# Performance work log

Hardware: AMD Instinct MI355X
Metric: run time of the kernel (lower is better)

Reference implementation:

```python
import jax, jax.numpy as jnp
import numpy as np

B, N_LEAVES, HID, NCLS, VOCAB = 32, 512, 128, 2, 50257
N_NODES = 2 * N_LEAVES - 1  # complete binary tree, heap layout


def setup_inputs() -> dict:
    key = jax.random.key(0)
    ks = jax.random.split(key, 12)
    x = jax.random.randint(ks[0], (B, N_NODES), 0, VOCAB)
    cue = jax.random.randint(ks[1], (B, N_NODES), 0, NCLS)
    # word j sits at tree leaf node L-1+j
    word_index = jnp.tile(jnp.arange(N_LEAVES - 1, 2 * N_LEAVES - 1), (B, 1))
    # parent->child adjacency stored in adj[:, 1]
    A = np.zeros((2, N_NODES, N_NODES), dtype=bool)
    p = np.arange(N_LEAVES - 1)
    A[1, p, 2 * p + 1] = True
    A[1, p, 2 * p + 2] = True
    adj = jnp.asarray(np.broadcast_to(A, (B, 2, N_NODES, N_NODES)).copy())
    s = 0.05
    emb = jax.random.normal(ks[2], (VOCAB, HID - NCLS)) * s
    Wc = jax.random.normal(ks[3], (HID, 2 * HID)) * s
    bc = jax.random.normal(ks[4], (HID,)) * s
    Wd = jax.random.normal(ks[5], (2 * HID, 2 * HID)) * s
    bd = jax.random.normal(ks[6], (2 * HID,)) * s
    Wg = jax.random.normal(ks[7], (HID, HID)) * s
    bg = jax.random.normal(ks[8], (HID,)) * s
    Wcl = jax.random.normal(ks[9], (NCLS, 2 * HID)) * s
    bcl = jax.random.normal(ks[10], (NCLS,)) * s
    return dict(x=x, word_index=word_index, cue=cue, adj=adj, emb=emb,
                Wc=Wc, bc=bc, Wd=Wd, bd=bd, Wg=Wg, bg=bg, Wcl=Wcl, bcl=bcl)


def reference(x, word_index, cue, adj, emb, Wc, bc, Wd, bd, Wg, bg, Wcl, bcl):
    # adj encodes the same complete binary heap tree that is hardcoded below
    Bn, N = x.shape
    H = Wc.shape[0]
    C = bcl.shape[0]
    L = (N + 1) // 2
    depth = L.bit_length() - 1  # leaves live at level `depth`
    bidx = jnp.arange(Bn)[:, None]

    word_emb = emb[x]                                   # (B, N, H-C)
    cue_oh = jax.nn.one_hot(cue, C, dtype=word_emb.dtype)
    in_feats = jnp.concatenate([word_emb, cue_oh], -1)  # (B, N, H)
    sent = in_feats[bidx, word_index]                   # (B, L, H) leaf feats

    # ---- upward compose: level-batched bottom-up traversal ----
    h = jnp.zeros((Bn, N, H), in_feats.dtype).at[bidx, word_index].set(sent)
    for d in range(depth - 1, -1, -1):
        p = jnp.arange(2 ** d - 1, 2 ** (d + 1) - 1)
        ctx = jnp.concatenate([h[:, 2 * p + 1], h[:, 2 * p + 2]], -1)  # (B, 2^d, 2H)
        h = h.at[:, p].set(jnp.tanh(ctx @ Wc.T + bc))
    # upward_results never writes leaf rows -> leaves stay zero
    up = h.at[bidx, word_index].set(0.0)

    g_down = jax.nn.sigmoid(h[:, 0] @ Wg.T + bg)        # (B, H)

    # ---- downward decompose: level-batched top-down traversal ----
    down = jnp.zeros_like(h).at[:, 0].set(g_down)
    for d in range(depth):
        p = jnp.arange(2 ** d - 1, 2 ** (d + 1) - 1)
        ctx = jnp.concatenate([down[:, p], up[:, p]], -1)
        ch = jnp.tanh(ctx @ Wd.T + bd)                  # (B, 2^d, 2H)
        down = down.at[:, 2 * p + 1].set(ch[..., :H]).at[:, 2 * p + 2].set(ch[..., H:])

    tree = jnp.concatenate([down, up], -1)              # (B, N, 2H)
    scores = jax.nn.sigmoid(tree @ Wcl.T + bcl)
    return jax.nn.softmax(scores, -1)
```

## Files before the change

kernel.cpp:

```cpp
#include <hip/hip_runtime.h>


constexpr int NNODES = 1023;
constexpr int HB = 128;

__device__ __forceinline__ float fold16(const float* a, int l) {
  float b[8];
#pragma unroll
  for (int u = 0; u < 8; ++u) {
    const float mine = (l & 1) ? a[2 * u + 1] : a[2 * u];
    const float oth  = (l & 1) ? a[2 * u]     : a[2 * u + 1];
    b[u] = mine + __shfl_xor(oth, 1);
  }
  float c[4];
#pragma unroll
  for (int u = 0; u < 4; ++u) {
    const float mine = (l & 2) ? b[2 * u + 1] : b[2 * u];
    const float oth  = (l & 2) ? b[2 * u]     : b[2 * u + 1];
    c[u] = mine + __shfl_xor(oth, 2);
  }
  float d[2];
#pragma unroll
  for (int u = 0; u < 2; ++u) {
    const float mine = (l & 4) ? c[2 * u + 1] : c[2 * u];
    const float oth  = (l & 4) ? c[2 * u]     : c[2 * u + 1];
    d[u] = mine + __shfl_xor(oth, 4);
  }
  const float mine = (l & 8) ? d[1] : d[0];
  const float oth  = (l & 8) ? d[0] : d[1];
  return mine + __shfl_xor(oth, 8);
}

__device__ __forceinline__ float fold8(const float* a, int l) {
  float b[4];
#pragma unroll
  for (int u = 0; u < 4; ++u) {
    const float mine = (l & 1) ? a[2 * u + 1] : a[2 * u];
    const float oth  = (l & 1) ? a[2 * u]     : a[2 * u + 1];
    b[u] = mine + __shfl_xor(oth, 1);
  }
  float c[2];
#pragma unroll
  for (int u = 0; u < 2; ++u) {
    const float mine = (l & 2) ? b[2 * u + 1] : b[2 * u];
    const float oth  = (l & 2) ? b[2 * u]     : b[2 * u + 1];
    c[u] = mine + __shfl_xor(oth, 2);
  }
  const float mine = (l & 4) ? c[1] : c[0];
  const float oth  = (l & 4) ? c[0] : c[1];
  return mine + __shfl_xor(oth, 4);
}

__device__ __forceinline__ float fold4(const float* a, int l) {
  float b[2];
#pragma unroll
  for (int u = 0; u < 2; ++u) {
    const float mine = (l & 1) ? a[2 * u + 1] : a[2 * u];
    const float oth  = (l & 1) ? a[2 * u]     : a[2 * u + 1];
    b[u] = mine + __shfl_xor(oth, 1);
  }
  const float mine = (l & 2) ? b[1] : b[0];
  const float oth  = (l & 2) ? b[0] : b[1];
  return mine + __shfl_xor(oth, 2);
}

template<int CH>
__device__ __forceinline__ float foldCH(const float (&a)[CH * 4], int l16) {
  if constexpr (CH == 4) {
    return fold16(a, l16);
  } else if constexpr (CH == 2) {
    float t = fold8(a, l16);
    t += __shfl_xor(t, 8);
    return t;
  } else {
    float t = fold4(a, l16);
    t += __shfl_xor(t, 4);
    t += __shfl_xor(t, 8);
    return t;
  }
}

template<int CH>
__device__ __forceinline__ void up_pass(float* __restrict__ heap, int base, int cb,
                                        int cbase, const float4 (&w)[4][4],
                                        float bias_r, int g, int l16, bool wr) {
  float2 a2[CH * 4];
#pragma unroll
  for (int v = 0; v < CH * 4; ++v) a2[v] = make_float2(0.f, 0.f);
#pragma unroll
  for (int p = 0; p < CH; ++p) {
    const float* cp = heap + (cb + 2 * (cbase + p)) * HB + l16 * 4;
#pragma unroll
    for (int m = 0; m < 4; ++m) {
      const float4 cc = *(const float4*)(cp + m * 64);
#pragma unroll
      for (int r = 0; r < 4; ++r) {
        const float4 wv = w[r][m];
        float2& av = a2[p * 4 + r];
        av.x = fmaf(wv.x, cc.x, av.x);
        av.y = fmaf(wv.y, cc.y, av.y);
        av.x = fmaf(wv.z, cc.z, av.x);
        av.y = fmaf(wv.w, cc.w, av.y);
      }
    }
  }
  float a[CH * 4];
#pragma unroll
  for (int v = 0; v < CH * 4; ++v) a[v] = a2[v].x + a2[v].y;
  const float tot = foldCH<CH>(a, l16);
  if (wr && l16 < CH * 4) {
    const int p = l16 >> 2;
    heap[(base + cbase + p) * HB + 4 * g + (l16 & 3)] = tanhf(tot + bias_r);
  }
}

template<int NP, int NH>
__device__ __forceinline__ void up_level16(float* __restrict__ heap,
                                           const float4 (&w)[4][4],
                                           float bias_r, int g, int l16, int ph) {
  constexpr int base = NP - 1, cb = 2 * NP - 1;
  if constexpr (NP >= 4 * NH) {
#pragma unroll
    for (int c0 = 0; c0 < NP; c0 += 4 * NH)
      up_pass<4>(heap, base, cb, c0 + ph * 4, w, bias_r, g, l16, true);
  } else if constexpr (NP * 2 == 4 * NH) {
    up_pass<2>(heap, base, cb, ph * 2, w, bias_r, g, l16, true);
  } else if constexpr (NP == NH) {
    up_pass<1>(heap, base, cb, ph, w, bias_r, g, l16, true);
  } else {
    up_pass<1>(heap, base, cb, 0, w, bias_r, g, l16, ph == 0);
  }
  __syncthreads();
}

template<int CH>
__device__ __forceinline__ void down_pass(float* __restrict__ db,
                                          const float* __restrict__ ub,
                                          int base, int cb, int cbase,
                                          const float4 (&w)[4][4],
                                          float bias_r, int g, int l16) {
  float2 a2[CH * 4];
#pragma unroll
  for (int v = 0; v < CH * 4; ++v) a2[v] = make_float2(0.f, 0.f);
#pragma unroll
  for (int p = 0; p < CH; ++p) {
    const float* dp = db + (base + cbase + p) * HB + l16 * 4;
    const float* up = ub + (base + cbase + p) * HB + l16 * 4;
#pragma unroll
    for (int m = 0; m < 4; ++m) {
      const float4 cc = *(const float4*)(((m < 2) ? dp : up) + (m & 1) * 64);
#pragma unroll
      for (int r = 0; r < 4; ++r) {
        const float4 wv = w[r][m];
        float2& av = a2[p * 4 + r];
        av.x = fmaf(wv.x, cc.x, av.x);
        av.y = fmaf(wv.y, cc.y, av.y);
        av.x = fmaf(wv.z, cc.z, av.x);
        av.y = fmaf(wv.w, cc.w, av.y);
      }
    }
  }
  float a[CH * 4];
#pragma unroll
  for (int v = 0; v < CH * 4; ++v) a[v] = a2[v].x + a2[v].y;
  const float tot = foldCH<CH>(a, l16);
  if (l16 < CH * 4) {
    const int p = l16 >> 2;
    const int row = 4 * g + (l16 & 3);
    db[(cb + 2 * (cbase + p) + (row >> 7)) * HB + (row & 127)] = tanhf(tot + bias_r);
  }
}

template<int NP>
__device__ __forceinline__ void down_level16(float* __restrict__ db,
                                             const float* __restrict__ ub,
                                             const float4 (&w)[4][4],
                                             float bias_r, int g, int l16) {
  constexpr int base = NP - 1, cb = 2 * NP - 1;
  if constexpr (NP >= 4) {
#pragma unroll
    for (int c0 = 0; c0 < NP; c0 += 4)
      down_pass<4>(db, ub, base, cb, c0, w, bias_r, g, l16);
  } else {
    down_pass<NP>(db, ub, base, cb, 0, w, bias_r, g, l16);
  }
  __syncthreads();
}

__device__ __forceinline__ void classify16(const float* __restrict__ dn,
                                           const float* __restrict__ un,
                                           const float* __restrict__ wcl,
                                           const float* __restrict__ bcl,
                                           float* __restrict__ o, int l16) {
  const int k0 = l16 * 8;
  float s0, s1;
  {
    const float4 d0 = *(const float4*)(dn + k0);
    const float4 d1 = *(const float4*)(dn + k0 + 4);
    const float4 a0 = *(const float4*)(wcl + k0);
    const float4 a1 = *(const float4*)(wcl + k0 + 4);
    const float4 b0 = *(const float4*)(wcl + 256 + k0);
    const float4 b1 = *(const float4*)(wcl + 256 + k0 + 4);
    s0 = d0.x * a0.x + d0.y * a0.y + d0.z * a0.z + d0.w * a0.w
       + d1.x * a1.x + d1.y * a1.y + d1.z * a1.z + d1.w * a1.w;
    s1 = d0.x * b0.x + d0.y * b0.y + d0.z * b0.z + d0.w * b0.w
       + d1.x * b1.x + d1.y * b1.y + d1.z * b1.z + d1.w * b1.w;
  }
  if (un) {
    const float4 u0 = *(const float4*)(un + k0);
    const float4 u1 = *(const float4*)(un + k0 + 4);
    const float4 a0 = *(const float4*)(wcl + 128 + k0);
    const float4 a1 = *(const float4*)(wcl + 128 + k0 + 4);
    const float4 b0 = *(const float4*)(wcl + 384 + k0);
    const float4 b1 = *(const float4*)(wcl + 384 + k0 + 4);
    s0 += u0.x * a0.x + u0.y * a0.y + u0.z * a0.z + u0.w * a0.w
        + u1.x * a1.x + u1.y * a1.y + u1.z * a1.z + u1.w * a1.w;
    s1 += u0.x * b0.x + u0.y * b0.y + u0.z * b0.z + u0.w * b0.w
        + u1.x * b1.x + u1.y * b1.y + u1.z * b1.z + u1.w * b1.w;
  }
#pragma unroll
  for (int m = 8; m >= 1; m >>= 1) {
    s0 += __shfl_xor(s0, m);
    s1 += __shfl_xor(s1, m);
  }
  if (l16 == 0) {
    s0 += bcl[0]; s1 += bcl[1];
    const float p0 = 1.f / (1.f + expf(-s0));
    const float p1 = 1.f / (1.f + expf(-s1));
    const float mx = fmaxf(p0, p1);
    const float e0 = expf(p0 - mx), e1 = expf(p1 - mx);
    const float inv = 1.f / (e0 + e1);
    o[0] = e0 * inv;
    o[1] = e1 * inv;
  }
}

__global__ __launch_bounds__(512, 4) void kA_up(const int* __restrict__ x,
                                                const int* __restrict__ cue,
                                                const float* __restrict__ emb,
                                                const float* __restrict__ Wc,
                                                const float* __restrict__ bc,
                                                float* __restrict__ hw) {
  __shared__ __align__(16) float heap[63 * HB];
  __shared__ __align__(16) float pad[7296];
  const int b = blockIdx.x >> 4, s = blockIdx.x & 15, r = 15 + s;
  const int t = threadIdx.x, g = t >> 4, l16 = t & 15;
  if (t == 0) ((volatile float*)pad)[0] = 0.f;

  float4 w[4][4];
#pragma unroll
  for (int rr = 0; rr < 4; ++rr)
#pragma unroll
    for (int m = 0; m < 4; ++m)
      w[rr][m] = *(const float4*)(Wc + (4 * g + rr) * 256 + l16 * 4 + m * 64);
  const float bias_r = bc[4 * g + (l16 & 3)];

  for (int idx = t; idx < 32 * HB; idx += 512) {
    const int j = idx >> 7, k = idx & 127;
    const int gq = ((r + 1) << 5) - 1 + j;
    float v;
    if (k < 126) v = emb[(long long)x[b * NNODES + gq] * 126 + k];
    else         v = (cue[b * NNODES + gq] == (k - 126)) ? 1.f : 0.f;
    heap[(31 + j) * HB + k] = v;
  }
  __syncthreads();

  up_level16<16, 1>(heap, w, bias_r, g, l16, 0);
  up_level16<8, 1>(heap, w, bias_r, g, l16, 0);
  up_level16<4, 1>(heap, w, bias_r, g, l16, 0);
  up_level16<2, 1>(heap, w, bias_r, g, l16, 0);
  up_level16<1, 1>(heap, w, bias_r, g, l16, 0);

  float4* dst = (float4*)(hw + (size_t)(b * 16 + s) * 31 * HB);
  const float4* src = (const float4*)heap;
  for (int idx = t; idx < 31 * 32; idx += 512) dst[idx] = src[idx];
}

__global__ __launch_bounds__(1024, 4) void kC_all(const float* __restrict__ Wc,
                                                  const float* __restrict__ bc,
                                                  const float* __restrict__ Wg,
                                                  const float* __restrict__ bg,
                                                  const float* __restrict__ Wd,
                                                  const float* __restrict__ bd,
                                                  const float* __restrict__ Wcl,
                                                  const float* __restrict__ bcl,
                                                  const float* __restrict__ hw,
                                                  float* __restrict__ out) {
  __shared__ __align__(16) float A[63 * HB];
  __shared__ __align__(16) float B[31 * HB];
  __shared__ __align__(16) float rootdn[2 * HB];
  __shared__ __align__(16) float wcl[512];
  __shared__ __align__(16) float pad[7400];
  const int b = blockIdx.x >> 3, sp = blockIdx.x & 7;
  const int t = threadIdx.x, g = t >> 4, l16 = t & 15;
  if (t == 0) ((volatile float*)pad)[0] = 0.f;

  {
    float4* B4 = (float4*)(B + 15 * HB);
    for (int idx = t; idx < 16 * 32; idx += 1024) {
      const int s = idx >> 5, k4 = idx & 31;
      B4[idx] = ((const float4*)(hw + (size_t)(b * 16 + s) * 31 * HB))[k4];
    }
  }
  if (t < 512) wcl[t] = Wcl[t];
  __syncthreads();

  {
    const int gu = g & 31, ph = t >> 9;
    float4 w[4][4];
#pragma unroll
    for (int rr = 0; rr < 4; ++rr)
#pragma unroll
      for (int m = 0; m < 4; ++m)
        w[rr][m] = *(const float4*)(Wc + (4 * gu + rr) * 256 + l16 * 4 + m * 64);
    const float bias_r = bc[4 * gu + (l16 & 3)];
    up_level16<8, 2>(B, w, bias_r, gu, l16, ph);
    up_level16<4, 2>(B, w, bias_r, gu, l16, ph);
    up_level16<2, 2>(B, w, bias_r, gu, l16, ph);
    up_level16<1, 2>(B, w, bias_r, gu, l16, ph);

    float4 wg[4][2];
#pragma unroll
    for (int rr = 0; rr < 4; ++rr)
#pragma unroll
      for (int m = 0; m < 2; ++m)
        wg[rr][m] = *(const float4*)(Wg + (4 * gu + rr) * 128 + l16 * 4 + m * 64);
    float a[4];
#pragma unroll
    for (int v = 0; v < 4; ++v) a[v] = 0.f;
#pragma unroll
    for (int m = 0; m < 2; ++m) {
      const float4 cc = *(const float4*)(B + l16 * 4 + m * 64);
#pragma unroll
      for (int rr = 0; rr < 4; ++rr) {
        const float4 wv = wg[rr][m];
        a[rr] = fmaf(wv.x, cc.x, fmaf(wv.y, cc.y, fmaf(wv.z, cc.z, fmaf(wv.w, cc.w, a[rr]))));
      }
    }
    float tot = fold4(a, l16);
    tot += __shfl_xor(tot, 4);
    tot += __shfl_xor(tot, 8);
    if (ph == 0 && l16 < 4) {
      const int row = 4 * gu + l16;
      A[row] = 1.f / (1.f + expf(-(tot + bg[row])));
    }
    __syncthreads();
  }
  asm volatile("" ::: "memory");

  float4 w[4][4];
#pragma unroll
  for (int rr = 0; rr < 4; ++rr)
#pragma unroll
    for (int m = 0; m < 4; ++m)
      w[rr][m] = *(const float4*)(Wd + (4 * g + rr) * 256 + l16 * 4 + m * 64);
  const float bias_r = bd[4 * g + (l16 & 3)];

  down_level16<1>(A, B, w, bias_r, g, l16);
  down_level16<2>(A, B, w, bias_r, g, l16);
  down_level16<4>(A, B, w, bias_r, g, l16);
  down_level16<8>(A, B, w, bias_r, g, l16);

  if (sp == 0 && t < 15 * 16) {
    const int m = t >> 4;
    classify16(A + m * HB, B + m * HB, wcl, bcl,
               out + ((size_t)b * NNODES + m) * 2, l16);
  }
  if (t < 256) rootdn[t] = A[(15 + sp * 2 + (t >> 7)) * HB + (t & 127)];
  __syncthreads();

  for (int ss = 0; ss < 2; ++ss) {
    const int s = sp * 2 + ss, r = 15 + s;

    {
      const float4* s4 = (const float4*)(hw + (size_t)(b * 16 + s) * 31 * HB);
      float4* B4 = (float4*)B;
      for (int idx = t; idx < 31 * 32; idx += 1024) B4[idx] = s4[idx];
      if (t < HB) A[t] = rootdn[ss * HB + t];
    }
    __syncthreads();

    down_level16<1>(A, B, w, bias_r, g, l16);
    down_level16<2>(A, B, w, bias_r, g, l16);
    down_level16<4>(A, B, w, bias_r, g, l16);
    down_level16<8>(A, B, w, bias_r, g, l16);
    down_level16<16>(A, B, w, bias_r, g, l16);

    if (t < 63 * 16) {
      const int m = t >> 4;
      const int lvl = 31 - __clz(m + 1);
      const int j = (m + 1) - (1 << lvl);
      const int gq = ((r + 1) << lvl) - 1 + j;
      classify16(A + m * HB, (m < 31) ? (B + m * HB) : nullptr, wcl, bcl,
                 out + ((size_t)b * NNODES + gq) * 2, l16);
    }
    __syncthreads();
  }
}

extern "C" void kernel_launch(void* const* d_in, const int* in_sizes, int n_in,
                              void* d_out, int out_size, void* d_ws, size_t ws_size,
                              hipStream_t stream) {
  const int*   x   = (const int*)d_in[0];
  const int*   cue = (const int*)d_in[2];
  const float* emb = (const float*)d_in[4];
  const float* Wc  = (const float*)d_in[5];
  const float* bc  = (const float*)d_in[6];
  const float* Wd  = (const float*)d_in[7];
  const float* bd  = (const float*)d_in[8];
  const float* Wg  = (const float*)d_in[9];
  const float* bg  = (const float*)d_in[10];
  const float* Wcl = (const float*)d_in[11];
  const float* bcl = (const float*)d_in[12];
  float* out = (float*)d_out;

  float* hw = (float*)d_ws;

  hipLaunchKernelGGL(kA_up,  dim3(512), dim3(512), 0, stream, x, cue, emb, Wc, bc, hw);
  hipLaunchKernelGGL(kC_all, dim3(256), dim3(1024), 0, stream,
                     Wc, bc, Wg, bg, Wd, bd, Wcl, bcl, hw, out);
}
```

Measured before the change: 79.81 us.

## Process both subtrees per block concurrently with dual shared buffers

The downward pass previously handled two subtrees one after the other, each level ending in its own barrier. Now both subtrees get their own A/B shared buffers, and each level runs down_pass on both before a single barrier, which halves the number of levels, barriers and reload phases. The padding array that deliberately inflated shared memory is removed, because the doubled buffers now take up that space. In exchange each thread does more work between barriers, and shared memory per block stays high.

```diff
diff --git a/kernel.cpp b/kernel.cpp
--- a/kernel.cpp
+++ b/kernel.cpp
@@ -183,6 +183,27 @@
       down_pass<4>(db, ub, base, cb, c0, w, bias_r, g, l16);
   } else {
     down_pass<NP>(db, ub, base, cb, 0, w, bias_r, g, l16);
+  }
+  __syncthreads();
+}
+
+template<int NP>
+__device__ __forceinline__ void down_level16_dual(float* __restrict__ A0,
+                                                  const float* __restrict__ B0,
+                                                  float* __restrict__ A1,
+                                                  const float* __restrict__ B1,
+                                                  const float4 (&w)[4][4],
+                                                  float bias_r, int g, int l16) {
+  constexpr int base = NP - 1, cb = 2 * NP - 1;
+  if constexpr (NP >= 4) {
+#pragma unroll
+    for (int c0 = 0; c0 < NP; c0 += 4) {
+      down_pass<4>(A0, B0, base, cb, c0, w, bias_r, g, l16);
+      down_pass<4>(A1, B1, base, cb, c0, w, bias_r, g, l16);
+    }
+  } else {
+    down_pass<NP>(A0, B0, base, cb, 0, w, bias_r, g, l16);
+    down_pass<NP>(A1, B1, base, cb, 0, w, bias_r, g, l16);
   }
   __syncthreads();
 }
@@ -286,14 +307,14 @@
                                                   const float* __restrict__ bcl,
                                                   const float* __restrict__ hw,
                                                   float* __restrict__ out) {
-  __shared__ __align__(16) float A[63 * HB];
-  __shared__ __align__(16) float B[31 * HB];
+  __shared__ __align__(16) float A[2 * 63 * HB];
+  __shared__ __align__(16) float B[2 * 31 * HB];
   __shared__ __align__(16) float rootdn[2 * HB];
   __shared__ __align__(16) float wcl[512];
-  __shared__ __align__(16) float pad[7400];
   const int b = blockIdx.x >> 3, sp = blockIdx.x & 7;
   const int t = threadIdx.x, g = t >> 4, l16 = t & 15;
-  if (t == 0) ((volatile float*)pad)[0] = 0.f;
+  float* A1 = A + 63 * HB;
+  float* B1 = B + 31 * HB;
 
   {
     float4* B4 = (float4*)(B + 15 * HB);
@@ -369,32 +390,35 @@
   if (t < 256) rootdn[t] = A[(15 + sp * 2 + (t >> 7)) * HB + (t & 127)];
   __syncthreads();
 
-  for (int ss = 0; ss < 2; ++ss) {
-    const int s = sp * 2 + ss, r = 15 + s;
-
-    {
-      const float4* s4 = (const float4*)(hw + (size_t)(b * 16 + s) * 31 * HB);
-      float4* B4 = (float4*)B;
-      for (int idx = t; idx < 31 * 32; idx += 1024) B4[idx] = s4[idx];
-      if (t < HB) A[t] = rootdn[ss * HB + t];
-    }
-    __syncthreads();
-
-    down_level16<1>(A, B, w, bias_r, g, l16);
-    down_level16<2>(A, B, w, bias_r, g, l16);
-    down_level16<4>(A, B, w, bias_r, g, l16);
-    down_level16<8>(A, B, w, bias_r, g, l16);
-    down_level16<16>(A, B, w, bias_r, g, l16);
-
-    if (t < 63 * 16) {
-      const int m = t >> 4;
-      const int lvl = 31 - __clz(m + 1);
-      const int j = (m + 1) - (1 << lvl);
+  {
+    for (int idx = t; idx < 2 * 31 * 32; idx += 1024) {
+      const int ss = (idx >= 31 * 32) ? 1 : 0;
+      const int k4 = idx - ss * 31 * 32;
+      ((float4*)(B + ss * 31 * HB))[k4] =
+          ((const float4*)(hw + (size_t)(b * 16 + sp * 2 + ss) * 31 * HB))[k4];
+    }
+    if (t < 256) A[(t >> 7) * 63 * HB + (t & 127)] = rootdn[t];
+  }
+  __syncthreads();
+
+  down_level16_dual<1>(A, B, A1, B1, w, bias_r, g, l16);
+  down_level16_dual<2>(A, B, A1, B1, w, bias_r, g, l16);
+  down_level16_dual<4>(A, B, A1, B1, w, bias_r, g, l16);
+  down_level16_dual<8>(A, B, A1, B1, w, bias_r, g, l16);
+  down_level16_dual<16>(A, B, A1, B1, w, bias_r, g, l16);
+
+  if (t < 63 * 16) {
+    const int m = t >> 4;
+    const int lvl = 31 - __clz(m + 1);
+    const int j = (m + 1) - (1 << lvl);
+#pragma unroll
+    for (int ss = 0; ss < 2; ++ss) {
+      const int r = 15 + sp * 2 + ss;
       const int gq = ((r + 1) << lvl) - 1 + j;
-      classify16(A + m * HB, (m < 31) ? (B + m * HB) : nullptr, wcl, bcl,
+      classify16(A + ss * 63 * HB + m * HB,
+                 (m < 31) ? (B + ss * 31 * HB + m * HB) : nullptr, wcl, bcl,
                  out + ((size_t)b * NNODES + gq) * 2, l16);
     }
-    __syncthreads();
   }
 }
 
```

New measurement: 77.80 us. 1.03x faster.
